# Kernel optimization log

Hardware: AMD Instinct MI355X
Metric: run time of the kernel (lower is better)

The kernel has to match this reference:

```python
import jax, jax.numpy as jnp
import numpy as np

N, E, IN, H, OUT = 100000, 1600000, 64, 64, 10
NEG_SLOPE = 0.2  # PyG GATConv default negative_slope


def _glorot(key, shape):
    fan = sum(shape) if len(shape) > 1 else shape[0]
    return jax.random.normal(key, shape, dtype=jnp.float32) * jnp.sqrt(2.0 / fan)


def setup_inputs() -> dict:
    key = jax.random.key(0)
    ks = jax.random.split(key, 16)
    x = jax.random.normal(ks[0], (N, IN), dtype=jnp.float32)
    edge_index = jax.random.randint(ks[1], (2, E), 0, N, dtype=jnp.int32)
    dims = [(IN, H), (H, H), (H, OUT)]
    params = {}
    for i, (fi, fo) in enumerate(dims, start=1):
        params[f"W{i}"] = _glorot(ks[4 * i - 2], (fi, fo))
        params[f"a{i}s"] = _glorot(ks[4 * i - 1], (fo,))
        params[f"a{i}d"] = _glorot(ks[4 * i], (fo,))
        params[f"b{i}"] = jnp.zeros((fo,), dtype=jnp.float32)
    return {"x": x, "edge_index": edge_index, **params}


def gat_conv(x, src, dst, W, a_s, a_d, b):
    """Single-head GATConv (PyG defaults): gather -> leaky_relu scores ->
    segment softmax over dst -> scatter-add aggregate."""
    n = x.shape[0]
    h = x @ W                                   # [N, Fo]
    alpha_src = h @ a_s                          # [N]
    alpha_dst = h @ a_d                          # [N]
    e = jax.nn.leaky_relu(alpha_src[src] + alpha_dst[dst], NEG_SLOPE)  # [E']
    m = jax.ops.segment_max(e, dst, num_segments=n)                    # stable softmax max
    ex = jnp.exp(e - m[dst])
    denom = jax.ops.segment_sum(ex, dst, num_segments=n)
    alpha = ex / denom[dst]                      # [E'] per-dst softmax
    out = jax.ops.segment_sum(alpha[:, None] * h[src], dst, num_segments=n)
    return out + b


def reference(x, edge_index, W1, a1s, a1d, b1, W2, a2s, a2d, b2, W3, a3s, a3d, b3):
    n = x.shape[0]
    loops = jnp.arange(n, dtype=edge_index.dtype)  # add_self_loops=True
    src = jnp.concatenate([edge_index[0], loops])
    dst = jnp.concatenate([edge_index[1], loops])
    h = jax.nn.relu(gat_conv(x, src, dst, W1, a1s, a1d, b1))
    # dropout is identity at inference (training=False)
    h = jax.nn.relu(gat_conv(h, src, dst, W2, a2s, a2d, b2))
    h = gat_conv(h, src, dst, W3, a3s, a3d, b3)
    return jax.nn.log_softmax(h, axis=1)
```

## Files before the change

### kernel.cpp

```cpp
#include <hip/hip_runtime.h>
#include <math.h>
#include <type_traits>


#define NEG_SLOPE 0.2f
#define BKT_BITS 9
#define BKT_SZ   512
#define PACK_SRC_BITS 20

typedef _Float16 h8v __attribute__((ext_vector_type(8)));
typedef _Float16 h4v __attribute__((ext_vector_type(4)));
typedef float f4v __attribute__((ext_vector_type(4)));

__global__ __launch_bounds__(512) void k_bscan(const int* __restrict__ bcount, int nb,
                                               int E, int N, int* __restrict__ ebase,
                                               int* __restrict__ gcur,
                                               int* __restrict__ rowptr) {
    __shared__ int sm[BKT_SZ];
    int t = threadIdx.x;
    int v = (t < nb) ? bcount[t] : 0;
    sm[t] = v;
    __syncthreads();
    for (int o = 1; o < BKT_SZ; o <<= 1) {
        int tv = (t >= o) ? sm[t - o] : 0;
        __syncthreads();
        sm[t] += tv;
        __syncthreads();
    }
    int excl = sm[t] - v;
    if (t < nb) {
        ebase[t] = excl;
        gcur[t] = excl;
    }
    if (t == nb - 1) ebase[nb] = excl + v;
    if (t == 0) rowptr[N] = E + N;
}

__global__ __launch_bounds__(1024) void k_bscatter(const int* __restrict__ src,
                                                   const int* __restrict__ dst, int E,
                                                   int nb, int* __restrict__ gcur,
                                                   int* __restrict__ ebuf) {
    __shared__ int lc[BKT_SZ];
    __shared__ int gb[BKT_SZ];
    for (int i = threadIdx.x; i < nb; i += 1024) lc[i] = 0;
    __syncthreads();
    int base = blockIdx.x * 8192;
    int bkt[8], rnk[8], pk[8];
#pragma unroll
    for (int j = 0; j < 8; j++) {
        int i = base + j * 1024 + threadIdx.x;
        bkt[j] = -1;
        if (i < E) {
            int d = dst[i];
            int s = src[i];
            int b = d >> BKT_BITS;
            bkt[j] = b;
            rnk[j] = atomicAdd(&lc[b], 1);
            pk[j] = ((d & (BKT_SZ - 1)) << PACK_SRC_BITS) | s;
        }
    }
    __syncthreads();
    for (int b = threadIdx.x; b < nb; b += 1024)
        if (lc[b]) gb[b] = atomicAdd(&gcur[b], lc[b]);
    __syncthreads();
#pragma unroll
    for (int j = 0; j < 8; j++)
        if (bkt[j] >= 0) ebuf[gb[bkt[j]] + rnk[j]] = pk[j];
}

__global__ __launch_bounds__(512) void k_bcsr(const int* __restrict__ ebuf,
                                              const int* __restrict__ ebase, int N,
                                              int* __restrict__ rowptr,
                                              int* __restrict__ csr) {
    __shared__ int cnt[BKT_SZ];
    __shared__ int sm[BKT_SZ];
    int b = blockIdx.x;
    int t = threadIdx.x;
    int n0 = b << BKT_BITS;
    int nn = min(BKT_SZ, N - n0);
    cnt[t] = 0;
    __syncthreads();
    int e0 = ebase[b], e1 = ebase[b + 1];
    for (int i = e0 + t; i < e1; i += BKT_SZ)
        atomicAdd(&cnt[ebuf[i] >> PACK_SRC_BITS], 1);
    __syncthreads();
    int v = cnt[t] + (t < nn ? 1 : 0);
    sm[t] = v;
    __syncthreads();
    for (int o = 1; o < BKT_SZ; o <<= 1) {
        int tv = (t >= o) ? sm[t - o] : 0;
        __syncthreads();
        sm[t] += tv;
        __syncthreads();
    }
    int excl = sm[t] - v;
    int cb = e0 + n0;
    if (t < nn) {
        rowptr[n0 + t] = cb + excl;
        csr[cb + excl] = n0 + t;
    }
    cnt[t] = excl + 1;
    __syncthreads();
    for (int i = e0 + t; i < e1; i += BKT_SZ) {
        int p = ebuf[i];
        int dl = p >> PACK_SRC_BITS;
        int pos = atomicAdd(&cnt[dl], 1);
        csr[cb + pos] = p & ((1 << PACK_SRC_BITS) - 1);
    }
}

__device__ __forceinline__ void gemm64_body(
    int bid, int nblocks, const float* __restrict__ X, const float* __restrict__ W,
    const float* __restrict__ a_s, const float* __restrict__ a_d, int N,
    _Float16* __restrict__ H, float* __restrict__ asb, float* __restrict__ adb) {
    constexpr int NT = 4;
    int lane = threadIdx.x & 63;
    int quad = lane >> 4;
    int c16 = lane & 15;

    h8v bf[NT][2];
    float asv[NT], adv[NT];
#pragma unroll
    for (int nt = 0; nt < NT; nt++) {
        int n = nt * 16 + c16;
        asv[nt] = a_s[n];
        adv[nt] = a_d[n];
#pragma unroll
        for (int kt = 0; kt < 2; kt++)
#pragma unroll
            for (int j = 0; j < 8; j++) {
                int k = kt * 32 + quad * 8 + j;
                bf[nt][kt][j] = (_Float16)W[k * 64 + n];
            }
    }

    int wid = (bid * 256 + (int)threadIdx.x) >> 6;
    int nw = (nblocks * 256) >> 6;
    int ntile = (N + 15) >> 4;

    for (int t = wid; t < ntile; t += nw) {
        int m0 = t << 4;
        int row = m0 + c16;
        const float* xr = X + (size_t)min(row, N - 1) * 64;
        h8v af[2];
#pragma unroll
        for (int kt = 0; kt < 2; kt++) {
            f4v x0 = *(const f4v*)(xr + kt * 32 + quad * 8);
            f4v x1 = *(const f4v*)(xr + kt * 32 + quad * 8 + 4);
#pragma unroll
            for (int j = 0; j < 4; j++) {
                af[kt][j] = (_Float16)x0[j];
                af[kt][4 + j] = (_Float16)x1[j];
            }
        }
        f4v c[NT];
#pragma unroll
        for (int nt = 0; nt < NT; nt++) c[nt] = (f4v){0.f, 0.f, 0.f, 0.f};
#pragma unroll
        for (int kt = 0; kt < 2; kt++)
#pragma unroll
            for (int nt = 0; nt < NT; nt++)
                c[nt] = __builtin_amdgcn_mfma_f32_16x16x32_f16(af[kt], bf[nt][kt],
                                                               c[nt], 0, 0, 0);
#pragma unroll
        for (int reg = 0; reg < 4; reg++) {
            int r = m0 + quad * 4 + reg;
            if (r < N) {
#pragma unroll
                for (int nt = 0; nt < NT; nt++)
                    H[(size_t)r * 64 + nt * 16 + c16] = (_Float16)c[nt][reg];
            }
        }
        float ps[4], pd[4];
#pragma unroll
        for (int reg = 0; reg < 4; reg++) {
            ps[reg] = 0.f;
            pd[reg] = 0.f;
#pragma unroll
            for (int nt = 0; nt < NT; nt++) {
                ps[reg] = fmaf(c[nt][reg], asv[nt], ps[reg]);
                pd[reg] = fmaf(c[nt][reg], adv[nt], pd[reg]);
            }
        }
        for (int o = 1; o < 16; o <<= 1) {
#pragma unroll
            for (int reg = 0; reg < 4; reg++) {
                ps[reg] += __shfl_xor(ps[reg], o, 64);
                pd[reg] += __shfl_xor(pd[reg], o, 64);
            }
        }
        if (c16 == 0) {
#pragma unroll
            for (int reg = 0; reg < 4; reg++) {
                int r = m0 + quad * 4 + reg;
                if (r < N) {
                    asb[r] = ps[reg];
                    adb[r] = pd[reg];
                }
            }
        }
    }
}

__global__ __launch_bounds__(256) void k_hist_gemm(
    const int* __restrict__ dst, int E, int nb, int* __restrict__ bcount,
    int histBlocks,
    const float* __restrict__ X, const float* __restrict__ W,
    const float* __restrict__ a_s, const float* __restrict__ a_d, int N,
    _Float16* __restrict__ H, float* __restrict__ asb, float* __restrict__ adb) {
    __shared__ int h[BKT_SZ];
    int bid = blockIdx.x;
    if (bid < histBlocks) {
        for (int i = threadIdx.x; i < nb; i += 256) h[i] = 0;
        __syncthreads();
        for (int i = bid * 256 + threadIdx.x; i < E; i += histBlocks * 256)
            atomicAdd(&h[dst[i] >> BKT_BITS], 1);
        __syncthreads();
        for (int i = threadIdx.x; i < nb; i += 256)
            if (h[i]) atomicAdd(&bcount[i], h[i]);
    } else {
        gemm64_body(bid - histBlocks, (int)gridDim.x - histBlocks, X, W, a_s, a_d,
                    N, H, asb, adb);
    }
}

template <int FP>
__global__ __launch_bounds__(256) void k_gemm(
    const float* __restrict__ X, const float* __restrict__ W,
    const float* __restrict__ a_s, const float* __restrict__ a_d,
    int N, int Freal,
    _Float16* __restrict__ H, float* __restrict__ asb, float* __restrict__ adb) {
    constexpr int NT = FP / 16;
    int lane = threadIdx.x & 63;
    int quad = lane >> 4;
    int c16 = lane & 15;

    h8v bf[NT][2];
    float asv[NT], adv[NT];
#pragma unroll
    for (int nt = 0; nt < NT; nt++) {
        int n = nt * 16 + c16;
        bool ok = (n < Freal);
        asv[nt] = ok ? a_s[n] : 0.f;
        adv[nt] = ok ? a_d[n] : 0.f;
#pragma unroll
        for (int kt = 0; kt < 2; kt++)
#pragma unroll
            for (int j = 0; j < 8; j++) {
                int k = kt * 32 + quad * 8 + j;
                bf[nt][kt][j] = (_Float16)(ok ? W[k * Freal + n] : 0.f);
            }
    }

    int wid = (blockIdx.x * blockDim.x + threadIdx.x) >> 6;
    int nw = (gridDim.x * blockDim.x) >> 6;
    int ntile = (N + 15) >> 4;

    for (int t = wid; t < ntile; t += nw) {
        int m0 = t << 4;
        int row = m0 + c16;
        const float* xr = X + (size_t)min(row, N - 1) * 64;
        h8v af[2];
#pragma unroll
        for (int kt = 0; kt < 2; kt++) {
            f4v x0 = *(const f4v*)(xr + kt * 32 + quad * 8);
            f4v x1 = *(const f4v*)(xr + kt * 32 + quad * 8 + 4);
#pragma unroll
            for (int j = 0; j < 4; j++) {
                af[kt][j] = (_Float16)x0[j];
                af[kt][4 + j] = (_Float16)x1[j];
            }
        }
        f4v c[NT];
#pragma unroll
        for (int nt = 0; nt < NT; nt++) c[nt] = (f4v){0.f, 0.f, 0.f, 0.f};
#pragma unroll
        for (int kt = 0; kt < 2; kt++)
#pragma unroll
            for (int nt = 0; nt < NT; nt++)
                c[nt] = __builtin_amdgcn_mfma_f32_16x16x32_f16(af[kt], bf[nt][kt],
                                                               c[nt], 0, 0, 0);
#pragma unroll
        for (int reg = 0; reg < 4; reg++) {
            int r = m0 + quad * 4 + reg;
            if (r < N) {
#pragma unroll
                for (int nt = 0; nt < NT; nt++)
                    H[(size_t)r * FP + nt * 16 + c16] = (_Float16)c[nt][reg];
            }
        }
        float ps[4], pd[4];
#pragma unroll
        for (int reg = 0; reg < 4; reg++) {
            ps[reg] = 0.f;
            pd[reg] = 0.f;
#pragma unroll
            for (int nt = 0; nt < NT; nt++) {
                ps[reg] = fmaf(c[nt][reg], asv[nt], ps[reg]);
                pd[reg] = fmaf(c[nt][reg], adv[nt], pd[reg]);
            }
        }
        for (int o = 1; o < 16; o <<= 1) {
#pragma unroll
            for (int reg = 0; reg < 4; reg++) {
                ps[reg] += __shfl_xor(ps[reg], o, 64);
                pd[reg] += __shfl_xor(pd[reg], o, 64);
            }
        }
        if (c16 == 0) {
#pragma unroll
            for (int reg = 0; reg < 4; reg++) {
                int r = m0 + quad * 4 + reg;
                if (r < N) {
                    asb[r] = ps[reg];
                    adb[r] = pd[reg];
                }
            }
        }
    }
}

template <int FP>
__device__ __forceinline__ void agg_slow(
    int node, const _Float16* __restrict__ H, const float* __restrict__ asb,
    const float* __restrict__ adb, const float* __restrict__ bias,
    const int* __restrict__ rowptr, const int* __restrict__ csr,
    int N, int Freal, float* __restrict__ out, int mode, int lane) {
    if (node >= N) return;
    int start = rowptr[node];
    int end = rowptr[node + 1];
    float ad = adb[node];
    int lf = lane & (FP - 1);
    const float NEG_INF = -__builtin_inff();

    float m = NEG_INF;
    for (int base = start; base < end; base += 64) {
        int i = base + lane;
        if (i < end) {
            float t = asb[csr[i]] + ad;
            float e = (t > 0.f) ? t : NEG_SLOPE * t;
            m = fmaxf(m, e);
        }
    }
    for (int o = 32; o > 0; o >>= 1) m = fmaxf(m, __shfl_xor(m, o, 64));
    float dsum = 0.f, acc = 0.f;
    for (int base = start; base < end; base += 64) {
        int i = base + lane;
        int cnt = min(64, end - base);
        int s = 0;
        float p = 0.f;
        if (i < end) {
            s = csr[i];
            float t = asb[s] + ad;
            float e = (t > 0.f) ? t : NEG_SLOPE * t;
            p = __expf(e - m);
        }
        dsum += p;
        for (int j = 0; j < cnt; j++) {
            float pj = __shfl(p, j, 64);
            int sj = __shfl(s, j, 64);
            acc = fmaf(pj, (float)H[(size_t)sj * FP + lf], acc);
        }
    }
    for (int o = 32; o > 0; o >>= 1) dsum += __shfl_xor(dsum, o, 64);

    float b = (lf < Freal) ? bias[lf] : 0.f;
    float z = acc / dsum + b;
    if (mode == 0) {
        if (lane < FP) out[(size_t)node * FP + lane] = fmaxf(z, 0.f);
    } else {
        float zz = (lane < Freal) ? z : NEG_INF;
        float zm = zz;
        for (int o = 32; o > 0; o >>= 1) zm = fmaxf(zm, __shfl_xor(zm, o, 64));
        float ez = (lane < Freal) ? __expf(zz - zm) : 0.f;
        float es = ez;
        for (int o = 32; o > 0; o >>= 1) es += __shfl_xor(es, o, 64);
        if (lane < Freal) out[(size_t)node * Freal + lane] = zz - zm - __logf(es);
    }
}

template <int FP, int W>
__global__ __launch_bounds__(256) void k_agg(
    const _Float16* __restrict__ H, const float* __restrict__ asb,
    const float* __restrict__ adb, const float* __restrict__ bias,
    const int* __restrict__ rowptr, const int* __restrict__ csr,
    int N, int Freal, float* __restrict__ out, int mode) {
    constexpr int LPR = FP / W;
    constexpr int GRPH = 32 / LPR;
    using vecW = typename std::conditional<W == 8, h8v, h4v>::type;
    int lane = threadIdx.x & 63;
    int half = lane >> 5;
    int li = lane & 31;
    int wid = (blockIdx.x * blockDim.x + threadIdx.x) >> 6;
    int nA = 2 * wid;
    if (nA >= N) return;
    int n = nA + half;
    bool valid = (n < N);
    int start = 0, end = 0;
    float ad = 0.f;
    if (valid) {
        start = rowptr[n];
        end = rowptr[n + 1];
        ad = adb[n];
    }
    int deg = end - start;
    int degm = max(deg, __shfl_xor(deg, 32, 64));

    const float NEG_INF = -__builtin_inff();

    if (degm <= 32) {
        int g = li / LPR;
        int fl = li % LPR;
        int s = 0;
        float e = NEG_INF;
        if (li < deg) {
            s = csr[start + li];
            float t = asb[s] + ad;
            e = (t > 0.f) ? t : NEG_SLOPE * t;
        }
        float m = e;
        for (int o = 16; o > 0; o >>= 1) m = fmaxf(m, __shfl_xor(m, o, 64));
        float p = (li < deg) ? __expf(e - m) : 0.f;
        float dsum = p;
        for (int o = 16; o > 0; o >>= 1) dsum += __shfl_xor(dsum, o, 64);

        float acc[W];
#pragma unroll
        for (int c = 0; c < W; c++) acc[c] = 0.f;
#pragma unroll 4
        for (int jb = 0; jb < degm; jb += GRPH) {
            int gidx = half * 32 + jb + g;
            float pj = __shfl(p, gidx, 64);
            int sj = __shfl(s, gidx, 64);
            vecW r = ((const vecW*)(H + (size_t)sj * FP))[fl];
#pragma unroll
            for (int c = 0; c < W; c++) acc[c] = fmaf(pj, (float)r[c], acc[c]);
        }
        for (int o = LPR; o < 32; o <<= 1) {
#pragma unroll
            for (int c = 0; c < W; c++) acc[c] += __shfl_xor(acc[c], o, 64);
        }
        float inv = 1.f / dsum;
        int fbase = fl * W;

        if (mode == 0) {
            if (valid && li < LPR) {
                float z[W];
#pragma unroll
                for (int c = 0; c < W; c++)
                    z[c] = fmaxf(fmaf(acc[c], inv, bias[fbase + c]), 0.f);
                float4* op = (float4*)(out + (size_t)n * FP + fbase);
#pragma unroll
                for (int q = 0; q < W / 4; q++)
                    op[q] = make_float4(z[4 * q], z[4 * q + 1], z[4 * q + 2],
                                        z[4 * q + 3]);
            }
        } else {
            float zc[W];
#pragma unroll
            for (int c = 0; c < W; c++) {
                int f = fbase + c;
                zc[c] = (f < Freal) ? fmaf(acc[c], inv, bias[f]) : NEG_INF;
            }
            float vm = zc[0];
#pragma unroll
            for (int c = 1; c < W; c++) vm = fmaxf(vm, zc[c]);
            for (int o = 1; o < LPR; o <<= 1) vm = fmaxf(vm, __shfl_xor(vm, o, 64));
            float es = 0.f;
#pragma unroll
            for (int c = 0; c < W; c++) es += __expf(zc[c] - vm);
            for (int o = 1; o < LPR; o <<= 1) es += __shfl_xor(es, o, 64);
            float ls = __logf(es);
            if (valid && li < LPR) {
#pragma unroll
                for (int c = 0; c < W; c++) {
                    int f = fbase + c;
                    if (f < Freal) out[(size_t)n * Freal + f] = zc[c] - vm - ls;
                }
            }
        }
    } else {
        agg_slow<FP>(nA, H, asb, adb, bias, rowptr, csr, N, Freal, out, mode, lane);
        agg_slow<FP>(nA + 1, H, asb, adb, bias, rowptr, csr, N, Freal, out, mode, lane);
    }
}

extern "C" void kernel_launch(void* const* d_in, const int* in_sizes, int n_in,
                              void* d_out, int out_size, void* d_ws, size_t ws_size,
                              hipStream_t stream) {
    const float* x = (const float*)d_in[0];
    const int* ei = (const int*)d_in[1];
    const float* W1 = (const float*)d_in[2];
    const float* a1s = (const float*)d_in[3];
    const float* a1d = (const float*)d_in[4];
    const float* b1 = (const float*)d_in[5];
    const float* W2 = (const float*)d_in[6];
    const float* a2s = (const float*)d_in[7];
    const float* a2d = (const float*)d_in[8];
    const float* b2 = (const float*)d_in[9];
    const float* W3 = (const float*)d_in[10];
    const float* a3s = (const float*)d_in[11];
    const float* a3d = (const float*)d_in[12];
    const float* b3 = (const float*)d_in[13];

    const int N = in_sizes[0] / 64;
    const int E = in_sizes[1] / 2;
    const int Etot = E + N;
    const int nb = (N + BKT_SZ - 1) >> BKT_BITS;
    const int* srcv = ei;
    const int* dstv = ei + E;

    size_t off = 0;
    char* base = (char*)d_ws;
    auto carve = [&](size_t bytes) -> void* {
        void* p = base + off;
        off = (off + bytes + 255) & ~(size_t)255;
        return p;
    };
    int* bcount = (int*)carve((size_t)(nb + 1) * 4);
    int* ebase = (int*)carve((size_t)(nb + 1) * 4);
    int* gcur = (int*)carve((size_t)nb * 4);
    int* rowptr = (int*)carve((size_t)(N + 1) * 4);
    int* csr = (int*)carve((size_t)Etot * 4);
    float* asb = (float*)carve((size_t)N * 4);
    float* adb = (float*)carve((size_t)N * 4);
    _Float16* hA = (_Float16*)carve((size_t)N * 64 * 2);
    float* fB = (float*)carve((size_t)N * 64 * 4);
    _Float16* hC = (_Float16*)carve((size_t)N * 16 * 2);
    int* ebuf = (int*)carve((size_t)E * 4);

    const int aggBlocks = (N + 7) / 8;
    const int gemmBlocks = 784;
    const int histBlocks = 512;

    hipMemsetAsync(bcount, 0, (size_t)nb * 4, stream);
    k_hist_gemm<<<histBlocks + gemmBlocks, 256, 0, stream>>>(
        dstv, E, nb, bcount, histBlocks, x, W1, a1s, a1d, N, hA, asb, adb);
    k_bscan<<<1, BKT_SZ, 0, stream>>>(bcount, nb, E, N, ebase, gcur, rowptr);
    k_bscatter<<<(E + 8191) / 8192, 1024, 0, stream>>>(srcv, dstv, E, nb, gcur, ebuf);
    k_bcsr<<<nb, BKT_SZ, 0, stream>>>(ebuf, ebase, N, rowptr, csr);

    k_agg<64, 8><<<aggBlocks, 256, 0, stream>>>(hA, asb, adb, b1, rowptr, csr, N, 64, fB, 0);
    k_gemm<64><<<gemmBlocks, 256, 0, stream>>>(fB, W2, a2s, a2d, N, 64, hA, asb, adb);
    k_agg<64, 8><<<aggBlocks, 256, 0, stream>>>(hA, asb, adb, b2, rowptr, csr, N, 64, fB, 0);
    k_gemm<16><<<gemmBlocks, 256, 0, stream>>>(fB, W3, a3s, a3d, N, 10, hC, asb, adb);
    k_agg<16, 4><<<aggBlocks, 256, 0, stream>>>(hC, asb, adb, b3, rowptr, csr, N, 10,
                                                (float*)d_out, 1);
}
```

Measured before the change: 329.5 us.

## Fuse layer-2 aggregation with layer-3 projection and fold bucket scan into consumers

Removes the single-block bucket scan kernel: k_bscatter and k_bcsr each recompute the prefix sum of bucket counts in shared memory, and gcur is zeroed and used as a relative cursor. Adds k_aggf, which aggregates layer 2, applies bias and ReLU, then multiplies by W3 and computes the layer-3 attention scalars in registers. This avoids writing the 64-wide fp32 fB intermediate and launching a separate gemm. The cost is redundant scans in every block, an extra memset, and heavier per-warp work in the fused kernel.

```diff
diff --git a/kernel.cpp b/kernel.cpp
--- a/kernel.cpp
+++ b/kernel.cpp
@@ -12,43 +12,23 @@
 typedef _Float16 h4v __attribute__((ext_vector_type(4)));
 typedef float f4v __attribute__((ext_vector_type(4)));
 
-__global__ __launch_bounds__(512) void k_bscan(const int* __restrict__ bcount, int nb,
-                                               int E, int N, int* __restrict__ ebase,
-                                               int* __restrict__ gcur,
-                                               int* __restrict__ rowptr) {
-    __shared__ int sm[BKT_SZ];
-    int t = threadIdx.x;
-    int v = (t < nb) ? bcount[t] : 0;
-    sm[t] = v;
-    __syncthreads();
-    for (int o = 1; o < BKT_SZ; o <<= 1) {
-        int tv = (t >= o) ? sm[t - o] : 0;
-        __syncthreads();
-        sm[t] += tv;
-        __syncthreads();
-    }
-    int excl = sm[t] - v;
-    if (t < nb) {
-        ebase[t] = excl;
-        gcur[t] = excl;
-    }
-    if (t == nb - 1) ebase[nb] = excl + v;
-    if (t == 0) rowptr[N] = E + N;
-}
-
 __global__ __launch_bounds__(1024) void k_bscatter(const int* __restrict__ src,
                                                    const int* __restrict__ dst, int E,
-                                                   int nb, int* __restrict__ gcur,
+                                                   int nb,
+                                                   const int* __restrict__ bcount,
+                                                   int* __restrict__ gcur,
                                                    int* __restrict__ ebuf) {
     __shared__ int lc[BKT_SZ];
     __shared__ int gb[BKT_SZ];
-    for (int i = threadIdx.x; i < nb; i += 1024) lc[i] = 0;
+    __shared__ int sc[BKT_SZ];
+    int t = threadIdx.x;
+    for (int i = t; i < nb; i += 1024) lc[i] = 0;
     __syncthreads();
     int base = blockIdx.x * 8192;
     int bkt[8], rnk[8], pk[8];
 #pragma unroll
     for (int j = 0; j < 8; j++) {
-        int i = base + j * 1024 + threadIdx.x;
+        int i = base + j * 1024 + t;
         bkt[j] = -1;
         if (i < E) {
             int d = dst[i];
@@ -60,8 +40,16 @@
         }
     }
     __syncthreads();
-    for (int b = threadIdx.x; b < nb; b += 1024)
-        if (lc[b]) gb[b] = atomicAdd(&gcur[b], lc[b]);
+    if (t < BKT_SZ) sc[t] = (t < nb) ? bcount[t] : 0;
+    __syncthreads();
+    for (int o = 1; o < BKT_SZ; o <<= 1) {
+        int tv = (t < BKT_SZ && t >= o) ? sc[t - o] : 0;
+        __syncthreads();
+        if (t < BKT_SZ) sc[t] += tv;
+        __syncthreads();
+    }
+    for (int b = t; b < nb; b += 1024)
+        if (lc[b]) gb[b] = (sc[b] - bcount[b]) + atomicAdd(&gcur[b], lc[b]);
     __syncthreads();
 #pragma unroll
     for (int j = 0; j < 8; j++)
@@ -69,18 +57,31 @@
 }
 
 __global__ __launch_bounds__(512) void k_bcsr(const int* __restrict__ ebuf,
-                                              const int* __restrict__ ebase, int N,
+                                              const int* __restrict__ bcount, int nb,
+                                              int E, int N,
                                               int* __restrict__ rowptr,
                                               int* __restrict__ csr) {
     __shared__ int cnt[BKT_SZ];
     __shared__ int sm[BKT_SZ];
     int b = blockIdx.x;
     int t = threadIdx.x;
+    sm[t] = (t < nb) ? bcount[t] : 0;
+    __syncthreads();
+    for (int o = 1; o < BKT_SZ; o <<= 1) {
+        int tv = (t >= o) ? sm[t - o] : 0;
+        __syncthreads();
+        sm[t] += tv;
+        __syncthreads();
+    }
+    int e1 = sm[b];
+    int e0 = e1 - bcount[b];
+    if (b == 0 && t == 0) rowptr[N] = E + N;
+    __syncthreads();
+
     int n0 = b << BKT_BITS;
     int nn = min(BKT_SZ, N - n0);
     cnt[t] = 0;
     __syncthreads();
-    int e0 = ebase[b], e1 = ebase[b + 1];
     for (int i = e0 + t; i < e1; i += BKT_SZ)
         atomicAdd(&cnt[ebuf[i] >> PACK_SRC_BITS], 1);
     __syncthreads();
@@ -377,6 +378,48 @@
         for (int o = 32; o > 0; o >>= 1) es += __shfl_xor(es, o, 64);
         if (lane < Freal) out[(size_t)node * Freal + lane] = zz - zm - __logf(es);
     }
+}
+
+__device__ __forceinline__ float agg_slow_z64(
+    int node, const _Float16* __restrict__ H, const float* __restrict__ asb,
+    const float* __restrict__ adb, const float* __restrict__ bias,
+    const int* __restrict__ rowptr, const int* __restrict__ csr, int lane) {
+    int start = rowptr[node];
+    int end = rowptr[node + 1];
+    float ad = adb[node];
+    const float NEG_INF = -__builtin_inff();
+
+    float m = NEG_INF;
+    for (int base = start; base < end; base += 64) {
+        int i = base + lane;
+        if (i < end) {
+            float t = asb[csr[i]] + ad;
+            float e = (t > 0.f) ? t : NEG_SLOPE * t;
+            m = fmaxf(m, e);
+        }
+    }
+    for (int o = 32; o > 0; o >>= 1) m = fmaxf(m, __shfl_xor(m, o, 64));
+    float dsum = 0.f, acc = 0.f;
+    for (int base = start; base < end; base += 64) {
+        int i = base + lane;
+        int cnt = min(64, end - base);
+        int s = 0;
+        float p = 0.f;
+        if (i < end) {
+            s = csr[i];
+            float t = asb[s] + ad;
+            float e = (t > 0.f) ? t : NEG_SLOPE * t;
+            p = __expf(e - m);
+        }
+        dsum += p;
+        for (int j = 0; j < cnt; j++) {
+            float pj = __shfl(p, j, 64);
+            int sj = __shfl(s, j, 64);
+            acc = fmaf(pj, (float)H[(size_t)sj * 64 + lane], acc);
+        }
+    }
+    for (int o = 32; o > 0; o >>= 1) dsum += __shfl_xor(dsum, o, 64);
+    return acc / dsum + bias[lane];
 }
 
 template <int FP, int W>
@@ -485,6 +528,154 @@
     }
 }
 
+__global__ __launch_bounds__(256) void k_aggf(
+    const _Float16* __restrict__ H, const float* __restrict__ asb,
+    const float* __restrict__ adb, const float* __restrict__ bias,
+    const int* __restrict__ rowptr, const int* __restrict__ csr, int N,
+    const float* __restrict__ W3, const float* __restrict__ a3s,
+    const float* __restrict__ a3d,
+    _Float16* __restrict__ H3, float* __restrict__ asb3,
+    float* __restrict__ adb3) {
+    constexpr int LPR = 8, GRPH = 4;
+    __shared__ float w3l[640];
+    __shared__ float a3sl[10], a3dl[10];
+    for (int i = threadIdx.x; i < 640; i += 256) w3l[i] = W3[i];
+    if (threadIdx.x < 10) {
+        a3sl[threadIdx.x] = a3s[threadIdx.x];
+        a3dl[threadIdx.x] = a3d[threadIdx.x];
+    }
+    __syncthreads();
+
+    int lane = threadIdx.x & 63;
+    int half = lane >> 5;
+    int li = lane & 31;
+    int wid = (blockIdx.x * blockDim.x + threadIdx.x) >> 6;
+    int nA = 2 * wid;
+    if (nA >= N) return;
+    int n = nA + half;
+    bool valid = (n < N);
+    int start = 0, end = 0;
+    float ad = 0.f;
+    if (valid) {
+        start = rowptr[n];
+        end = rowptr[n + 1];
+        ad = adb[n];
+    }
+    int deg = end - start;
+    int degm = max(deg, __shfl_xor(deg, 32, 64));
+
+    const float NEG_INF = -__builtin_inff();
+
+    if (degm <= 32) {
+        int g = li / LPR;
+        int fl = li % LPR;
+        int s = 0;
+        float e = NEG_INF;
+        if (li < deg) {
+            s = csr[start + li];
+            float t = asb[s] + ad;
+            e = (t > 0.f) ? t : NEG_SLOPE * t;
+        }
+        float m = e;
+        for (int o = 16; o > 0; o >>= 1) m = fmaxf(m, __shfl_xor(m, o, 64));
+        float p = (li < deg) ? __expf(e - m) : 0.f;
+        float dsum = p;
+        for (int o = 16; o > 0; o >>= 1) dsum += __shfl_xor(dsum, o, 64);
+
+        float acc[8];
+#pragma unroll
+        for (int c = 0; c < 8; c++) acc[c] = 0.f;
+#pragma unroll 4
+        for (int jb = 0; jb < degm; jb += GRPH) {
+            int gidx = half * 32 + jb + g;
+            float pj = __shfl(p, gidx, 64);
+            int sj = __shfl(s, gidx, 64);
+            h8v r = ((const h8v*)(H + (size_t)sj * 64))[fl];
+#pragma unroll
+            for (int c = 0; c < 8; c++) acc[c] = fmaf(pj, (float)r[c], acc[c]);
+        }
+        for (int o = LPR; o < 32; o <<= 1) {
+#pragma unroll
+            for (int c = 0; c < 8; c++) acc[c] += __shfl_xor(acc[c], o, 64);
+        }
+        float inv = 1.f / dsum;
+        int fbase = fl * 8;
+        float z[8];
+#pragma unroll
+        for (int c = 0; c < 8; c++)
+            z[c] = fmaxf(fmaf(acc[c], inv, bias[fbase + c]), 0.f);
+        float pt[10];
+#pragma unroll
+        for (int t = 0; t < 10; t++) pt[t] = 0.f;
+#pragma unroll
+        for (int c = 0; c < 8; c++) {
+            const float* wr = &w3l[(fbase + c) * 10];
+            float zv = z[c];
+#pragma unroll
+            for (int t = 0; t < 10; t++) pt[t] = fmaf(zv, wr[t], pt[t]);
+        }
+        for (int o = 1; o < 8; o <<= 1) {
+#pragma unroll
+            for (int t = 0; t < 10; t++) pt[t] += __shfl_xor(pt[t], o, 64);
+        }
+        if (valid) {
+            if (li == 0) {
+                h8v hv;
+#pragma unroll
+                for (int j = 0; j < 8; j++) hv[j] = (_Float16)pt[j];
+                *(h8v*)(H3 + (size_t)n * 16) = hv;
+                float s3 = 0.f, d3 = 0.f;
+#pragma unroll
+                for (int t = 0; t < 10; t++) {
+                    s3 = fmaf(pt[t], a3sl[t], s3);
+                    d3 = fmaf(pt[t], a3dl[t], d3);
+                }
+                asb3[n] = s3;
+                adb3[n] = d3;
+            }
+            if (li == 8) {
+                h8v hv2 = {};
+                hv2[0] = (_Float16)pt[8];
+                hv2[1] = (_Float16)pt[9];
+                *(h8v*)(H3 + (size_t)n * 16 + 8) = hv2;
+            }
+        }
+    } else {
+        for (int q = 0; q < 2; q++) {
+            int node = nA + q;
+            if (node >= N) continue;
+            float z = agg_slow_z64(node, H, asb, adb, bias, rowptr, csr, lane);
+            z = fmaxf(z, 0.f);
+            float pt[10];
+            const float* wr = &w3l[lane * 10];
+#pragma unroll
+            for (int t = 0; t < 10; t++) pt[t] = z * wr[t];
+            for (int o = 1; o < 64; o <<= 1) {
+#pragma unroll
+                for (int t = 0; t < 10; t++) pt[t] += __shfl_xor(pt[t], o, 64);
+            }
+            if (lane == 0) {
+                h8v hv;
+#pragma unroll
+                for (int j = 0; j < 8; j++) hv[j] = (_Float16)pt[j];
+                *(h8v*)(H3 + (size_t)node * 16) = hv;
+                h8v hv2 = {};
+                hv2[0] = (_Float16)pt[8];
+                hv2[1] = (_Float16)pt[9];
+                *(h8v*)(H3 + (size_t)node * 16 + 8) = hv2;
+                float s3 = 0.f, d3 = 0.f;
+#pragma unroll
+                for (int t = 0; t < 10; t++) {
+                    s3 = fmaf(pt[t], a3sl[t], s3);
+                    d3 = fmaf(pt[t], a3dl[t], d3);
+                }
+                asb3[node] = s3;
+                adb3[node] = d3;
+            }
+        }
+    }
+}
+
 extern "C" void kernel_launch(void* const* d_in, const int* in_sizes, int n_in,
                               void* d_out, int out_size, void* d_ws, size_t ws_size,
                               hipStream_t stream) {
@@ -518,12 +709,13 @@
         return p;
     };
     int* bcount = (int*)carve((size_t)(nb + 1) * 4);
-    int* ebase = (int*)carve((size_t)(nb + 1) * 4);
     int* gcur = (int*)carve((size_t)nb * 4);
     int* rowptr = (int*)carve((size_t)(N + 1) * 4);
     int* csr = (int*)carve((size_t)Etot * 4);
     float* asb = (float*)carve((size_t)N * 4);
     float* adb = (float*)carve((size_t)N * 4);
+    float* asb3 = (float*)carve((size_t)N * 4);
+    float* adb3 = (float*)carve((size_t)N * 4);
     _Float16* hA = (_Float16*)carve((size_t)N * 64 * 2);
     float* fB = (float*)carve((size_t)N * 64 * 4);
     _Float16* hC = (_Float16*)carve((size_t)N * 16 * 2);
@@ -534,16 +726,17 @@
     const int histBlocks = 512;
 
     hipMemsetAsync(bcount, 0, (size_t)nb * 4, stream);
+    hipMemsetAsync(gcur, 0, (size_t)nb * 4, stream);
     k_hist_gemm<<<histBlocks + gemmBlocks, 256, 0, stream>>>(
         dstv, E, nb, bcount, histBlocks, x, W1, a1s, a1d, N, hA, asb, adb);
-    k_bscan<<<1, BKT_SZ, 0, stream>>>(bcount, nb, E, N, ebase, gcur, rowptr);
-    k_bscatter<<<(E + 8191) / 8192, 1024, 0, stream>>>(srcv, dstv, E, nb, gcur, ebuf);
-    k_bcsr<<<nb, BKT_SZ, 0, stream>>>(ebuf, ebase, N, rowptr, csr);
+    k_bscatter<<<(E + 8191) / 8192, 1024, 0, stream>>>(srcv, dstv, E, nb, bcount,
+                                                       gcur, ebuf);
+    k_bcsr<<<nb, BKT_SZ, 0, stream>>>(ebuf, bcount, nb, E, N, rowptr, csr);
 
     k_agg<64, 8><<<aggBlocks, 256, 0, stream>>>(hA, asb, adb, b1, rowptr, csr, N, 64, fB, 0);
     k_gemm<64><<<gemmBlocks, 256, 0, stream>>>(fB, W2, a2s, a2d, N, 64, hA, asb, adb);
-    k_agg<64, 8><<<aggBlocks, 256, 0, stream>>>(hA, asb, adb, b2, rowptr, csr, N, 64, fB, 0);
-    k_gemm<16><<<gemmBlocks, 256, 0, stream>>>(fB, W3, a3s, a3d, N, 10, hC, asb, adb);
-    k_agg<16, 4><<<aggBlocks, 256, 0, stream>>>(hC, asb, adb, b3, rowptr, csr, N, 10,
-                                                (float*)d_out, 1);
-}
+    k_aggf<<<aggBlocks, 256, 0, stream>>>(hA, asb, adb, b2, rowptr, csr, N, W3,
+                                          a3s, a3d, hC, asb3, adb3);
+    k_agg<16, 4><<<aggBlocks, 256, 0, stream>>>(hC, asb3, adb3, b3, rowptr, csr,
+                                                N, 10, (float*)d_out, 1);
+}
```

Measured after the change: 336.0 us. About the same (+2.0%).
